# Kernel optimization log

Measured on AMD Instinct MI355X. Metric: run time of the kernel, lower is better.

## Reference

```python
import jax, jax.numpy as jnp
import numpy as np

KEEP_RATIO = 0.5
TEMPERATURE = 1.0
MIN_GATE = 0.0
EPS = 1e-06


def setup_inputs() -> dict:
    key = jax.random.key(0)
    k1, k2 = jax.random.split(key)
    B, C = 8192, 4096
    token = jax.random.normal(k1, (B, C), dtype=jnp.float32)
    proxy = jax.random.normal(k2, (B, C), dtype=jnp.float32)
    return {"token": token, "proxy": proxy}


def reference(token, proxy):
    tok = token  # [B, C]
    px = jax.lax.stop_gradient(proxy)  # detach_proxy=True
    score = jnp.abs(tok * px)  # [B, C]
    B, C = score.shape
    k = max(1, int(round(C * KEEP_RATIO)))
    # hard mask: top-k indices per row -> scatter 1.0
    _, topk_idx = jax.lax.top_k(score, k)  # [B, k]
    rows = jnp.arange(B)[:, None]
    hard_mask = jnp.zeros_like(score).at[rows, topk_idx].set(1.0)
    # per-row standardization (torch.std is unbiased -> ddof=1)
    mu = jnp.mean(score, axis=-1, keepdims=True)
    sigma = jnp.maximum(jnp.std(score, axis=-1, ddof=1, keepdims=True), EPS)
    z = (score - mu) / sigma / max(TEMPERATURE, EPS)
    soft_gate = jax.nn.sigmoid(z)
    if MIN_GATE > 0:
        soft_gate = soft_gate * (1.0 - MIN_GATE) + MIN_GATE
    gate = soft_gate * (1.0 - hard_mask) + hard_mask
    return tok * gate
```

## Files before the change

kernel.cpp:

```cpp
#include <hip/hip_runtime.h>
#include <math.h>

#define CLS   4096
#define KSEL  2048u
#define TPB   256

typedef float f32x4 __attribute__((ext_vector_type(4)));


__device__ __forceinline__ int h0slot(unsigned b) {
    unsigned j = b & 7u, t = b >> 3;
    return (int)((j << 8) | ((t + 4u*j) & 255u));
}

template<int SHIFT, int NBITS, int BPL>
__device__ __forceinline__ void radix_small(const float sc[16], unsigned* hist,
        int lane, unsigned& prefix, unsigned& kr, unsigned& cnt_eq)
{
    const unsigned msk = (1u << NBITS) - 1u;
    #pragma unroll
    for (int i = 0; i < 16; ++i) {
        unsigned u = __float_as_uint(sc[i]);
        if ((u >> (SHIFT + NBITS)) == (prefix >> (SHIFT + NBITS)))
            atomicAdd(&hist[(u >> SHIFT) & msk], 1u);
    }
    __syncthreads();
    unsigned c[BPL];
    if constexpr (BPL == 4) {
        uint4 x = *(const uint4*)&hist[lane * 4];
        c[0] = x.x; c[1] = x.y; c[2] = x.z; c[3] = x.w;
    } else {
        c[0] = hist[lane];
    }
    unsigned sfx[BPL + 1]; sfx[BPL] = 0;
    #pragma unroll
    for (int j = BPL - 1; j >= 0; --j) sfx[j] = sfx[j + 1] + c[j];
    const unsigned tot = sfx[0];
    unsigned s = tot;
    #pragma unroll
    for (int off = 1; off < 64; off <<= 1) {
        unsigned t = __shfl_down(s, off);
        if (lane + off < 64) s += t;
    }
    const unsigned Sx = s - tot;
    const bool has = (Sx < kr) && (kr <= Sx + tot);
    unsigned bin = 0, below = 0, ceq = 0;
    if (has) {
        #pragma unroll
        for (int j = 0; j < BPL; ++j)
            if (Sx + sfx[j] >= kr && Sx + sfx[j + 1] < kr) {
                bin = (unsigned)(lane * BPL + j);
                below = Sx + sfx[j + 1];
                ceq = c[j];
            }
    }
    unsigned long long m = __ballot(has);
    int src = (int)__builtin_ctzll(m);
    bin = __shfl(bin, src); below = __shfl(below, src); ceq = __shfl(ceq, src);
    prefix |= bin << SHIFT;
    kr -= below;
    cnt_eq = ceq;
}

template<int K>
__device__ __forceinline__ unsigned ballot_sel(const unsigned* cand, unsigned cnt,
                                               unsigned kr, int lane)
{
    unsigned key[K]; unsigned long long m[K];
    #pragma unroll
    for (int w = 0; w < K; ++w) {
        unsigned base = (unsigned)w * 64u;
        bool v = (base + (unsigned)lane) < cnt;
        key[w] = v ? cand[base + lane] : 0u;
        unsigned rem = (cnt > base) ? (cnt - base) : 0u;
        m[w] = (rem >= 64u) ? ~0ull : ((rem == 0u) ? 0ull : ((1ull << rem) - 1ull));
    }
    unsigned Kstar = 0u;
    #pragma unroll
    for (int b = 31; b >= 0; --b) {
        unsigned long long t[K];
        unsigned c1 = 0;
        #pragma unroll
        for (int w = 0; w < K; ++w) {
            t[w] = m[w] & __ballot((key[w] >> b) & 1u);
            c1 += (unsigned)__popcll(t[w]);
        }
        if (c1 >= kr) {
            #pragma unroll
            for (int w = 0; w < K; ++w) m[w] = t[w];
            Kstar |= (1u << b);
        } else {
            kr -= c1;
            #pragma unroll
            for (int w = 0; w < K; ++w) m[w] &= ~t[w];
        }
    }
    return Kstar;
}

__global__ __launch_bounds__(TPB) void proxy_gate_kernel(
    const float* __restrict__ token,
    const float* __restrict__ proxy,
    float* __restrict__ out)
{
    __shared__ __align__(16) unsigned char lds[18816];
    unsigned* h0    = (unsigned*)(lds);
    unsigned* cand  = (unsigned*)(lds + 16416);
    unsigned* h1    = (unsigned*)(lds + 16416);
    unsigned* h2    = (unsigned*)(lds + 17456);
    unsigned* h3    = (unsigned*)(lds + 18496);
    unsigned* s_cnt = (unsigned*)(lds + 18752);
    unsigned* s_wt  = (unsigned*)(lds + 18756);
    unsigned* s_bc  = (unsigned*)(lds + 18772);
    float*    s_fr  = (float*)   (lds + 18784);
    unsigned char* s_flag = lds;
    unsigned*      s_suf  = (unsigned*)(lds + 8192);

    const int tid  = threadIdx.x;
    const int lane = tid & 63;
    const int wv   = tid >> 6;
    const size_t base = (size_t)blockIdx.x * CLS;
    const float4* t4 = (const float4*)(token + base);
    const float4* p4 = (const float4*)(proxy + base);
    f32x4* o4 = (f32x4*)(out + base);

    float4 tv[4], pv[4];
    #pragma unroll
    for (int i = 0; i < 4; ++i) { tv[i] = t4[i*TPB + tid]; pv[i] = p4[i*TPB + tid]; }
    {
        uint4 z = make_uint4(0u, 0u, 0u, 0u);
        uint4* zp = (uint4*)lds;
        #pragma unroll
        for (int m = 0; m < 5; ++m) { int idx = m*TPB + tid; if (idx < 1026) zp[idx] = z; }
        if (tid == 0) *s_cnt = 0u;
    }

    float tok[16], sc[16];
    float sum = 0.f, sumsq = 0.f;
    #pragma unroll
    for (int i = 0; i < 4; ++i) {
        float a;
        a = fabsf(tv[i].x*pv[i].x); tok[i*4+0]=tv[i].x; sc[i*4+0]=a; sum+=a; sumsq+=a*a;
        a = fabsf(tv[i].y*pv[i].y); tok[i*4+1]=tv[i].y; sc[i*4+1]=a; sum+=a; sumsq+=a*a;
        a = fabsf(tv[i].z*pv[i].z); tok[i*4+2]=tv[i].z; sc[i*4+2]=a; sum+=a; sumsq+=a*a;
        a = fabsf(tv[i].w*pv[i].w); tok[i*4+3]=tv[i].w; sc[i*4+3]=a; sum+=a; sumsq+=a*a;
    }
    __syncthreads();

    {
        unsigned* h0c = h0 + (((tid >> 2) & 1) ? 2052 : 0);
        #pragma unroll
        for (int i = 0; i < 16; ++i)
            atomicAdd(&h0c[h0slot(__float_as_uint(sc[i]) >> 20)], 1u);
    }
    #pragma unroll
    for (int off = 32; off > 0; off >>= 1) {
        sum   += __shfl_xor(sum, off);
        sumsq += __shfl_xor(sumsq, off);
    }
    if (lane == 0) { s_fr[wv] = sum; s_fr[4+wv] = sumsq; }
    __syncthreads();

    const float tot_s = s_fr[0]+s_fr[1]+s_fr[2]+s_fr[3];
    const float tot_q = s_fr[4]+s_fr[5]+s_fr[6]+s_fr[7];
    const float mu = tot_s * (1.0f/CLS);
    float var = (tot_q - tot_s*mu) * (1.0f/(CLS-1));
    var = fmaxf(var, 0.0f);
    const float inv_sigma = 1.0f / fmaxf(sqrtf(var), 1e-6f);

    unsigned kr = KSEL, cnt_eq = 0;
    {
        unsigned c[8];
        #pragma unroll
        for (int j = 0; j < 8; ++j) {
            int sl = (j << 8) | ((tid + 4*j) & 255);
            c[j] = h0[sl] + h0[2052 + sl];
        }
        unsigned sfx[9]; sfx[8] = 0;
        #pragma unroll
        for (int j = 7; j >= 0; --j) sfx[j] = sfx[j+1] + c[j];
        const unsigned tot = sfx[0];
        unsigned s = tot;
        #pragma unroll
        for (int off = 1; off < 64; off <<= 1) {
            unsigned t = __shfl_down(s, off);
            if (lane + off < 64) s += t;
        }
        if (lane == 0) s_wt[wv] = s;
        __syncthreads();
        unsigned addhi = 0;
        #pragma unroll
        for (int w2 = 0; w2 < 4; ++w2) if (w2 > wv) addhi += s_wt[w2];
        const unsigned Sx = (s - tot) + addhi;
        if (Sx < kr && kr <= Sx + tot) {
            #pragma unroll
            for (int j = 0; j < 8; ++j)
                if (Sx + sfx[j] >= kr && Sx + sfx[j+1] < kr) {
                    s_bc[0] = (unsigned)(tid*8 + j);
                    s_bc[1] = Sx + sfx[j+1];
                    s_bc[2] = c[j];
                }
        }
        __syncthreads();
        kr    -= s_bc[1];
        cnt_eq = s_bc[2];
    }
    const unsigned bin = s_bc[0];

    {
        unsigned wtot = 0;
        #pragma unroll
        for (int ii = 0; ii < 16; ++ii) {
            bool cnd = ((__float_as_uint(sc[ii]) >> 20) == bin);
            wtot += (unsigned)__popcll(__ballot(cnd));
        }
        unsigned wbase = 0;
        if (lane == 0) wbase = atomicAdd(s_cnt, wtot);
        wbase = __shfl(wbase, 0);
        unsigned run = wbase;
        #pragma unroll
        for (int ii = 0; ii < 16; ++ii) {
            unsigned u = __float_as_uint(sc[ii]);
            bool cnd = ((u >> 20) == bin);
            unsigned long long mm = __ballot(cnd);
            if (cnd) {
                unsigned pos = run + (unsigned)__popcll(mm & ((1ull << lane) - 1ull));
                unsigned idx = (unsigned)((ii >> 2)*1024 + tid*4 + (ii & 3));
                if (pos < 256u) cand[pos] = ((u & 0xFFFFFu) << 12) | (4095u - idx);
            }
            run += (unsigned)__popcll(mm);
        }
    }
    __syncthreads();
    const unsigned cnt = *s_cnt;
    const bool ballot_mode = (cnt <= 256u);

    unsigned Kstar = 0;
    float thr = 0.f; bool tie_rare = false; unsigned prefix = bin << 20;
    if (ballot_mode) {
        Kstar = (cnt <= 128u) ? ballot_sel<2>(cand, cnt, kr, lane)
                              : ballot_sel<4>(cand, cnt, kr, lane);
    } else {
        {
            unsigned* hz = (unsigned*)(lds + 16416);
            #pragma unroll
            for (int m = 0; m < 3; ++m) { int ix = m*TPB + tid; if (ix < 584) hz[ix] = 0u; }
        }
        __syncthreads();
        radix_small<12, 8, 4>(sc, h1, lane, prefix, kr, cnt_eq);
        radix_small< 4, 8, 4>(sc, h2, lane, prefix, kr, cnt_eq);
        radix_small< 0, 4, 1>(sc, h3, lane, prefix, kr, cnt_eq);
        thr = __uint_as_float(prefix);
        tie_rare = (cnt_eq != kr);
        if (tie_rare) {
            #pragma unroll
            for (int i = 0; i < 4; ++i)
                #pragma unroll
                for (int c2 = 0; c2 < 4; ++c2)
                    s_flag[i*1024 + tid*4 + c2] = (sc[i*4+c2] == thr) ? 1 : 0;
            __syncthreads();
            unsigned lc = 0;
            unsigned char mf[16];
            #pragma unroll
            for (int m = 0; m < 16; ++m) { mf[m] = s_flag[tid*16 + m]; lc += mf[m]; }
            s_suf[tid] = lc;
            __syncthreads();
            #pragma unroll
            for (int off = 1; off < 256; off <<= 1) {
                unsigned w = s_suf[tid] + ((tid >= off) ? s_suf[tid - off] : 0u);
                __syncthreads();
                s_suf[tid] = w;
                __syncthreads();
            }
            unsigned r = s_suf[tid] - lc;
            #pragma unroll
            for (int m = 0; m < 16; ++m) {
                if (mf[m]) { s_flag[tid*16 + m] = (r < kr) ? 2 : 0; ++r; }
            }
            __syncthreads();
        }
    }

    #pragma unroll
    for (int i = 0; i < 4; ++i) {
        float res[4];
        #pragma unroll
        for (int c2 = 0; c2 < 4; ++c2) {
            const float s = sc[i*4+c2];
            const float z = (s - mu) * inv_sigma;
            const float soft = 1.0f / (1.0f + __expf(-z));
            bool hard;
            const unsigned u = __float_as_uint(s);
            if (ballot_mode) {
                const unsigned e = u >> 20;
                const unsigned idx = (unsigned)(i*1024 + tid*4 + c2);
                const unsigned packed = ((u & 0xFFFFFu) << 12) | (4095u - idx);
                hard = (e > bin) || ((e == bin) && (packed >= Kstar));
            } else if (tie_rare) {
                hard = (s > thr) || ((s == thr) && (s_flag[i*1024 + tid*4 + c2] == 2));
            } else {
                hard = (s >= thr);
            }
            res[c2] = tok[i*4+c2] * (hard ? 1.0f : soft);
        }
        f32x4 rv = { res[0], res[1], res[2], res[3] };
        __builtin_nontemporal_store(rv, &o4[i*TPB + tid]);
    }
}

extern "C" void kernel_launch(void* const* d_in, const int* in_sizes, int n_in,
                              void* d_out, int out_size, void* d_ws, size_t ws_size,
                              hipStream_t stream) {
    const float* token = (const float*)d_in[0];
    const float* proxy = (const float*)d_in[1];
    float* outp = (float*)d_out;
    const int B = in_sizes[0] / CLS;
    hipLaunchKernelGGL(proxy_gate_kernel, dim3(B), dim3(TPB), 0, stream,
                       token, proxy, outp);
}
```

Baseline: 75.52 us.

## Replace ballot bitwise selection with rank-counting over candidates up to 512

Replaces the 32-step wave-ballot radix selection over the candidate list with an all-pairs rank count: each thread takes one or two candidates, counts how many candidates are larger, and the one whose rank equals kr-1 writes the kth key to shared memory. Candidate compaction now uses a per-thread bitmask plus a wave prefix scan instead of 16 ballots. The candidate buffer grows to 512 entries so the histogram-refinement fallback is needed less often. In exchange, each thread does O(cnt) LDS reads per candidate and more shared memory is zeroed.

```diff
diff --git a/kernel.cpp b/kernel.cpp
--- a/kernel.cpp
+++ b/kernel.cpp
@@ -60,42 +60,6 @@
     prefix |= bin << SHIFT;
     kr -= below;
     cnt_eq = ceq;
-}
-
-template<int K>
-__device__ __forceinline__ unsigned ballot_sel(const unsigned* cand, unsigned cnt,
-                                               unsigned kr, int lane)
-{
-    unsigned key[K]; unsigned long long m[K];
-    #pragma unroll
-    for (int w = 0; w < K; ++w) {
-        unsigned base = (unsigned)w * 64u;
-        bool v = (base + (unsigned)lane) < cnt;
-        key[w] = v ? cand[base + lane] : 0u;
-        unsigned rem = (cnt > base) ? (cnt - base) : 0u;
-        m[w] = (rem >= 64u) ? ~0ull : ((rem == 0u) ? 0ull : ((1ull << rem) - 1ull));
-    }
-    unsigned Kstar = 0u;
-    #pragma unroll
-    for (int b = 31; b >= 0; --b) {
-        unsigned long long t[K];
-        unsigned c1 = 0;
-        #pragma unroll
-        for (int w = 0; w < K; ++w) {
-            t[w] = m[w] & __ballot((key[w] >> b) & 1u);
-            c1 += (unsigned)__popcll(t[w]);
-        }
-        if (c1 >= kr) {
-            #pragma unroll
-            for (int w = 0; w < K; ++w) m[w] = t[w];
-            Kstar |= (1u << b);
-        } else {
-            kr -= c1;
-            #pragma unroll
-            for (int w = 0; w < K; ++w) m[w] &= ~t[w];
-        }
-    }
-    return Kstar;
 }
 
 __global__ __launch_bounds__(TPB) void proxy_gate_kernel(
@@ -131,7 +95,7 @@
         uint4 z = make_uint4(0u, 0u, 0u, 0u);
         uint4* zp = (uint4*)lds;
         #pragma unroll
-        for (int m = 0; m < 5; ++m) { int idx = m*TPB + tid; if (idx < 1026) zp[idx] = z; }
+        for (int m = 0; m < 5; ++m) { int idx = m*TPB + tid; if (idx < 1154) zp[idx] = z; }
         if (tid == 0) *s_cnt = 0u;
     }
 
@@ -168,7 +132,7 @@
     var = fmaxf(var, 0.0f);
     const float inv_sigma = 1.0f / fmaxf(sqrtf(var), 1e-6f);
 
-    unsigned kr = KSEL, cnt_eq = 0;
+    unsigned kr = KSEL;
     {
         unsigned c[8];
         #pragma unroll
@@ -202,45 +166,64 @@
                 }
         }
         __syncthreads();
-        kr    -= s_bc[1];
-        cnt_eq = s_bc[2];
+        kr -= s_bc[1];
     }
     const unsigned bin = s_bc[0];
+    unsigned cnt_eq = s_bc[2];
 
     {
-        unsigned wtot = 0;
+        unsigned cmask = 0, lc = 0;
         #pragma unroll
         for (int ii = 0; ii < 16; ++ii) {
             bool cnd = ((__float_as_uint(sc[ii]) >> 20) == bin);
-            wtot += (unsigned)__popcll(__ballot(cnd));
-        }
+            cmask |= ((unsigned)cnd) << ii;
+            lc += (unsigned)cnd;
+        }
+        unsigned inc = lc;
+        #pragma unroll
+        for (int off = 1; off < 64; off <<= 1) {
+            unsigned t = __shfl_up(inc, off);
+            if (lane >= off) inc += t;
+        }
+        const unsigned wtot = __shfl(inc, 63);
         unsigned wbase = 0;
         if (lane == 0) wbase = atomicAdd(s_cnt, wtot);
         wbase = __shfl(wbase, 0);
-        unsigned run = wbase;
+        unsigned p = wbase + (inc - lc);
         #pragma unroll
         for (int ii = 0; ii < 16; ++ii) {
-            unsigned u = __float_as_uint(sc[ii]);
-            bool cnd = ((u >> 20) == bin);
-            unsigned long long mm = __ballot(cnd);
-            if (cnd) {
-                unsigned pos = run + (unsigned)__popcll(mm & ((1ull << lane) - 1ull));
+            if ((cmask >> ii) & 1u) {
+                unsigned u = __float_as_uint(sc[ii]);
                 unsigned idx = (unsigned)((ii >> 2)*1024 + tid*4 + (ii & 3));
-                if (pos < 256u) cand[pos] = ((u & 0xFFFFFu) << 12) | (4095u - idx);
-            }
-            run += (unsigned)__popcll(mm);
+                if (p < 512u) cand[p] = ((u & 0xFFFFFu) << 12) | (4095u - idx);
+                ++p;
+            }
         }
     }
     __syncthreads();
     const unsigned cnt = *s_cnt;
-    const bool ballot_mode = (cnt <= 256u);
-
-    unsigned Kstar = 0;
-    float thr = 0.f; bool tie_rare = false; unsigned prefix = bin << 20;
-    if (ballot_mode) {
-        Kstar = (cnt <= 128u) ? ballot_sel<2>(cand, cnt, kr, lane)
-                              : ballot_sel<4>(cand, cnt, kr, lane);
+    const bool cand_mode = (cnt <= 512u);
+
+    float thr = 0.f; bool tie_rare = false;
+    if (cand_mode) {
+        #pragma unroll
+        for (int rpt = 0; rpt < 2; ++rpt) {
+            const unsigned slot = (unsigned)tid + (unsigned)rpt*256u;
+            if (slot < cnt) {
+                const unsigned my = cand[slot];
+                unsigned rank = 0;
+                const uint4* c4 = (const uint4*)cand;
+                const unsigned nq = (cnt + 3u) >> 2;
+                for (unsigned q = 0; q < nq; ++q) {
+                    uint4 v = c4[q];
+                    rank += (unsigned)(v.x > my) + (unsigned)(v.y > my)
+                          + (unsigned)(v.z > my) + (unsigned)(v.w > my);
+                }
+                if (rank == kr - 1u) s_bc[0] = my;
+            }
+        }
     } else {
+        unsigned prefix = bin << 20;
         {
             unsigned* hz = (unsigned*)(lds + 16416);
             #pragma unroll
@@ -277,9 +260,10 @@
             for (int m = 0; m < 16; ++m) {
                 if (mf[m]) { s_flag[tid*16 + m] = (r < kr) ? 2 : 0; ++r; }
             }
-            __syncthreads();
-        }
-    }
+        }
+    }
+    __syncthreads();
+    const unsigned Kth = s_bc[0];
 
     #pragma unroll
     for (int i = 0; i < 4; ++i) {
@@ -291,11 +275,11 @@
             const float soft = 1.0f / (1.0f + __expf(-z));
             bool hard;
             const unsigned u = __float_as_uint(s);
-            if (ballot_mode) {
+            if (cand_mode) {
                 const unsigned e = u >> 20;
                 const unsigned idx = (unsigned)(i*1024 + tid*4 + c2);
                 const unsigned packed = ((u & 0xFFFFFu) << 12) | (4095u - idx);
-                hard = (e > bin) || ((e == bin) && (packed >= Kstar));
+                hard = (e > bin) || ((e == bin) && (packed >= Kth));
             } else if (tie_rare) {
                 hard = (s > thr) || ((s == thr) && (s_flag[i*1024 + tid*4 + c2] == 2));
             } else {
```

Measured after the change: 72.65 us. 3.8% less time.
